# Kernel optimization log

Hardware: AMD Instinct MI355X
Metric: run time of the kernel (lower is better)

Reference implementation:

```python
import jax, jax.numpy as jnp
import numpy as np

VOCAB = 50001  # vocab_size + 1
EMB = 64
HID = 128
TAGS = 32
B, T = 256, 512


def setup_inputs() -> dict:
    key = jax.random.key(0)
    ks = jax.random.split(key, 12)
    inputs = jax.random.randint(ks[0], (B, T), 0, VOCAB)
    labels = jax.random.randint(ks[1], (B, T), 0, TAGS)
    E = jax.random.normal(ks[2], (VOCAB, EMB), jnp.float32) * 0.1
    def glorot(k, shape):
        fan = sum(shape)
        return jax.random.uniform(k, shape, jnp.float32, -1.0, 1.0) * jnp.sqrt(6.0 / fan)
    Wk_f = glorot(ks[3], (EMB, 4 * HID))
    Wr_f = glorot(ks[4], (HID, 4 * HID))
    b_f = jnp.zeros((4 * HID,), jnp.float32)
    Wk_b = glorot(ks[5], (EMB, 4 * HID))
    Wr_b = glorot(ks[6], (HID, 4 * HID))
    b_b = jnp.zeros((4 * HID,), jnp.float32)
    Wd = glorot(ks[7], (2 * HID, TAGS))
    bd = jnp.zeros((TAGS,), jnp.float32)
    transition = jax.random.uniform(ks[8], (TAGS, TAGS), jnp.float32)
    return {"inputs": inputs, "labels": labels, "E": E,
            "Wk_f": Wk_f, "Wr_f": Wr_f, "b_f": b_f,
            "Wk_b": Wk_b, "Wr_b": Wr_b, "b_b": b_b,
            "Wd": Wd, "bd": bd, "transition": transition}


def _lstm(x, Wk, Wr, b, reverse):
    # x: (B, T, D) -> (B, T, H); Keras gate order i, f, g(cell), o
    Bb = x.shape[0]
    H = Wr.shape[0]
    xs = jnp.swapaxes(x, 0, 1)  # (T, B, D)

    def step(carry, xt):
        h, c = carry
        z = xt @ Wk + h @ Wr + b
        i, f, g, o = jnp.split(z, 4, axis=-1)
        c = jax.nn.sigmoid(f) * c + jax.nn.sigmoid(i) * jnp.tanh(g)
        h = jax.nn.sigmoid(o) * jnp.tanh(c)
        return (h, c), h

    init = (jnp.zeros((Bb, H), x.dtype), jnp.zeros((Bb, H), x.dtype))
    _, hs = jax.lax.scan(step, init, xs, reverse=reverse)
    return jnp.swapaxes(hs, 0, 1)  # (B, T, H), time-aligned for both directions


def _crf_log_likelihood(logits, labels, transition):
    # logits: (B, T, K), labels: (B, T) int, full-length sequences
    lt = jnp.swapaxes(logits, 0, 1)  # (T, B, K)

    def fstep(alpha, lg):
        # alpha: (B, K) -> logsumexp over previous tag
        alpha = jax.nn.logsumexp(alpha[:, :, None] + transition[None], axis=1) + lg
        return alpha, None

    alpha, _ = jax.lax.scan(fstep, lt[0], lt[1:])
    log_norm = jax.nn.logsumexp(alpha, axis=-1)  # (B,)
    unary = jnp.take_along_axis(logits, labels[..., None], axis=-1)[..., 0].sum(-1)
    binary = transition[labels[:, :-1], labels[:, 1:]].sum(-1)
    return unary + binary - log_norm


def reference(inputs, labels, E, Wk_f, Wr_f, b_f, Wk_b, Wr_b, b_b, Wd, bd, transition):
    emb = E[inputs]  # (B, T, EMB) embedding lookup
    h_f = _lstm(emb, Wk_f, Wr_f, b_f, reverse=False)
    h_b = _lstm(emb, Wk_b, Wr_b, b_b, reverse=True)
    h = jnp.concatenate([h_f, h_b], axis=-1)  # (B, T, 2H)
    logits = h @ Wd + bd  # (B, T, K)
    log_likelihood = _crf_log_likelihood(logits, labels, transition)
    return log_likelihood, transition
```

## Files before the change

### kernel.cpp

```cpp
#include <hip/hip_runtime.h>
#include <hip/hip_bf16.h>
#include <cstdint>
#include <cstddef>

#define VOCAB 50001
#define EMB 64
#define HID 128
#define G4  512
#define TAGS 32
#define BATCH 256
#define SEQ 512

typedef _Float16 f16;
typedef _Float16 f16x2 __attribute__((ext_vector_type(2)));
typedef _Float16 f16x4 __attribute__((ext_vector_type(4)));
typedef _Float16 f16x8 __attribute__((ext_vector_type(8)));
typedef float f32x4 __attribute__((ext_vector_type(4)));

__device__ __forceinline__ float rcpf(float x) { return __builtin_amdgcn_rcpf(x); }

#define MFMA16(A, B, C) __builtin_amdgcn_mfma_f32_16x16x32_f16((A), (B), (C), 0, 0, 0)

__global__ __launch_bounds__(256)
void gtab_mfma_kernel(const float* __restrict__ E,
                      const float* __restrict__ Wk_f, const float* __restrict__ b_f,
                      const float* __restrict__ Wk_b, const float* __restrict__ b_b,
                      f16* __restrict__ G_f, f16* __restrict__ G_b) {
  const int dir = blockIdx.z;
  const float* __restrict__ Wk   = dir ? Wk_b : Wk_f;
  const float* __restrict__ bias = dir ? b_b  : b_f;
  f16* __restrict__ G = dir ? G_b : G_f;

  const int m0 = blockIdx.x * 64;
  const int n0 = blockIdx.y * 256;
  const int tid = threadIdx.x;

  __shared__ f16 Eh[64][80];
  __shared__ f16 Bh[256][80];

  #pragma unroll
  for (int s = 0; s < 4; ++s) {
    int idx = tid + s * 256;
    int r = idx >> 4, c4 = (idx & 15) * 4;
    int row = m0 + r;
    float4 ev;
    if (row < VOCAB) ev = *(const float4*)(E + (size_t)row * EMB + c4);
    else { ev.x = 0.f; ev.y = 0.f; ev.z = 0.f; ev.w = 0.f; }
    f16x4 v; v[0] = (f16)ev.x; v[1] = (f16)ev.y; v[2] = (f16)ev.z; v[3] = (f16)ev.w;
    *(f16x4*)&Eh[r][c4] = v;
  }
  #pragma unroll
  for (int s = 0; s < 32; ++s) {
    int idx = tid + s * 256;
    int k = idx >> 7, n2 = (idx & 127) * 2;
    float2 wv = *(const float2*)(Wk + (size_t)k * G4 + n0 + n2);
    Bh[n2][k]     = (f16)wv.x;
    Bh[n2 + 1][k] = (f16)wv.y;
  }
  __syncthreads();

  const int w = tid >> 6, l = tid & 63, mn = l & 15, q = l >> 4;
  f16x8 a0 = *(const f16x8*)&Eh[16 * w + mn][8 * q];
  f16x8 a1 = *(const f16x8*)&Eh[16 * w + mn][32 + 8 * q];

  f32x4 acc[16];
  #pragma unroll
  for (int nt = 0; nt < 16; ++nt) {
    f16x8 b0 = *(const f16x8*)&Bh[16 * nt + mn][8 * q];
    f16x8 b1 = *(const f16x8*)&Bh[16 * nt + mn][32 + 8 * q];
    f32x4 z = {0.f, 0.f, 0.f, 0.f};
    z = MFMA16(a0, b0, z);
    z = MFMA16(a1, b1, z);
    acc[nt] = z;
  }

  const int gA = n0 >> 7;
  #pragma unroll
  for (int nt = 0; nt < 8; ++nt) {
    int hid = 16 * nt + mn;
    float bv0 = bias[n0 + 16 * nt + mn];
    float bv1 = bias[n0 + 128 + 16 * nt + mn];
    #pragma unroll
    for (int reg = 0; reg < 4; ++reg) {
      int row = m0 + 16 * w + 4 * q + reg;
      if (row < VOCAB) {
        f16x2 v; v.x = (f16)(acc[nt][reg] + bv0); v.y = (f16)(acc[nt + 8][reg] + bv1);
        *(f16x2*)(G + (size_t)row * G4 + hid * 4 + gA) = v;
      }
    }
  }
}

__global__ __launch_bounds__(512, 1)
void lstm_mfma_kernel(const int* __restrict__ tokens,
                      const f16* __restrict__ G_f, const f16* __restrict__ G_b,
                      const float* __restrict__ Wr_f, const float* __restrict__ Wr_b,
                      const float* __restrict__ Wd, const float* __restrict__ bd,
                      float* __restrict__ Lf, float* __restrict__ Lb) {
  const int bg  = blockIdx.x;
  const int dir = blockIdx.y;
  const int b0  = bg * 2;
  const f16* __restrict__ G = dir ? G_b : G_f;
  const float* __restrict__ Wr = dir ? Wr_b : Wr_f;
  float* __restrict__ Lout = dir ? Lb : Lf;

  const int tid = threadIdx.x;
  const int w = tid >> 6;
  const int l = tid & 63;
  const int mn = l & 15;
  const int q  = l >> 4;
  const int hid = 16 * w + mn;

  __shared__ __align__(16) f16 h_lds[2][2][160];
  __shared__ int tokT[SEQ][2];

  tokT[tid][0] = tokens[(size_t)(b0 + 0) * SEQ + tid];
  tokT[tid][1] = tokens[(size_t)(b0 + 1) * SEQ + tid];
  if (tid < 160) ((unsigned*)&h_lds[0][0][0])[tid] = 0u;

  f16x8 bw[4][4];
  #pragma unroll
  for (int g = 0; g < 4; ++g) {
    #pragma unroll
    for (int s = 0; s < 4; ++s) {
      f16x8 v;
      const int colv = 128 * g + hid;
      #pragma unroll
      for (int j = 0; j < 8; ++j)
        v[j] = (f16)Wr[(size_t)(32 * s + 8 * q + j) * G4 + colv];
      bw[g][s] = v;
    }
  }
  f16x8 wdf0{}, wdf1{}, wdf2{}, wdf3{};
  float bdv = 0.0f;
  if (w >= 6) {
    const int tag = 16 * (w - 6) + mn;
    #pragma unroll
    for (int j = 0; j < 8; ++j) {
      wdf0[j] = (f16)Wd[(size_t)(128 * dir +  0 + 8 * q + j) * TAGS + tag];
      wdf1[j] = (f16)Wd[(size_t)(128 * dir + 32 + 8 * q + j) * TAGS + tag];
      wdf2[j] = (f16)Wd[(size_t)(128 * dir + 64 + 8 * q + j) * TAGS + tag];
      wdf3[j] = (f16)Wd[(size_t)(128 * dir + 96 + 8 * q + j) * TAGS + tag];
    }
    if (dir == 0) bdv = bd[tag];
  }

  float cst = 0.0f;
  __syncthreads();

#define TT(S) (dir ? (SEQ - 1 - (S)) : (S))

#define LOADG(S, GV) do { if (l < 32) {                                        \
    int _tk = tokT[TT(S)][q];                                                  \
    GV = *(const uint2*)(G + (size_t)_tk * G4 + hid * 4); } } while (0)

#define STEP(S, GV) do {                                                       \
    const int _s = (S);                                                        \
    const int _t = TT(_s);                                                     \
    const f16* hb = &h_lds[_s & 1][mn & 1][0];                                 \
    f16x8 a0 = *(const f16x8*)(hb      + 8 * q);                               \
    f16x8 a1 = *(const f16x8*)(hb + 32 + 8 * q);                               \
    f16x8 a2 = *(const f16x8*)(hb + 64 + 8 * q);                               \
    f16x8 a3 = *(const f16x8*)(hb + 96 + 8 * q);                               \
    f32x4 z0 = {0.f,0.f,0.f,0.f}, z1 = {0.f,0.f,0.f,0.f};                      \
    f32x4 z2 = {0.f,0.f,0.f,0.f}, z3 = {0.f,0.f,0.f,0.f};                      \
    z0 = MFMA16(a0, bw[0][0], z0); z0 = MFMA16(a1, bw[0][1], z0);              \
    z0 = MFMA16(a2, bw[0][2], z0); z0 = MFMA16(a3, bw[0][3], z0);              \
    z1 = MFMA16(a0, bw[1][0], z1); z1 = MFMA16(a1, bw[1][1], z1);              \
    z1 = MFMA16(a2, bw[1][2], z1); z1 = MFMA16(a3, bw[1][3], z1);              \
    z2 = MFMA16(a0, bw[2][0], z2); z2 = MFMA16(a1, bw[2][1], z2);              \
    z2 = MFMA16(a2, bw[2][2], z2); z2 = MFMA16(a3, bw[2][3], z2);              \
    z3 = MFMA16(a0, bw[3][0], z3); z3 = MFMA16(a1, bw[3][1], z3);              \
    z3 = MFMA16(a2, bw[3][2], z3); z3 = MFMA16(a3, bw[3][3], z3);              \
    if (w >= 6) {                                                              \
      f32x4 la = {0.f,0.f,0.f,0.f};                                            \
      la = MFMA16(a0, wdf0, la); la = MFMA16(a1, wdf1, la);                    \
      la = MFMA16(a2, wdf2, la); la = MFMA16(a3, wdf3, la);                    \
      if (q == 0) {                                                            \
        const int tag = 16 * (w - 6) + mn;                                     \
        Lout[((size_t)(b0 + 0) * SEQ + _t) * TAGS + tag] = la[0] + bdv;        \
        Lout[((size_t)(b0 + 1) * SEQ + _t) * TAGS + tag] = la[1] + bdv;        \
      }                                                                        \
    }                                                                          \
    float s0 = __shfl(z0[1], mn);                                              \
    float s1 = __shfl(z1[1], mn);                                              \
    float s2 = __shfl(z2[1], mn);                                              \
    float s3 = __shfl(z3[1], mn);                                              \
    if (l < 32) {                                                              \
      float zi = q ? s0 : z0[0];                                               \
      float zf = q ? s1 : z1[0];                                               \
      float zg = q ? s2 : z2[0];                                               \
      float zo = q ? s3 : z3[0];                                               \
      f16x4 gv = __builtin_bit_cast(f16x4, GV);                                \
      zi += (float)gv[0]; zf += (float)gv[1];                                  \
      zg += (float)gv[2]; zo += (float)gv[3];                                  \
      float ei = __expf(-zi);                                                  \
      float eg = __expf(fminf(2.f * zg, 30.f));                                \
      float sab = (eg - 1.f) * rcpf((1.f + ei) * (eg + 1.f));                  \
      float ef = __expf(-zf);                                                  \
      float cc = rcpf(1.f + ef) * cst + sab;                                   \
      cst = cc;                                                                \
      float eo = __expf(-zo);                                                  \
      float ec = __expf(fminf(2.f * cc, 30.f));                                \
      float hh = (ec - 1.f) * rcpf((1.f + eo) * (ec + 1.f));                   \
      h_lds[(_s + 1) & 1][q][hid] = (f16)hh;                                   \
    }                                                                          \
    asm volatile("s_waitcnt lgkmcnt(0)" ::: "memory");                         \
    __builtin_amdgcn_s_barrier();                                              \
  } while (0)

  uint2 gA, gB, gC, gD;
  LOADG(0, gA); LOADG(1, gB); LOADG(2, gC); LOADG(3, gD);

  for (int it = 0; it < SEQ / 4; ++it) {
    const int s = 4 * it;
    STEP(s + 0, gA);
    { int sc = (s + 4 < SEQ) ? s + 4 : SEQ - 1; LOADG(sc, gA); }
    STEP(s + 1, gB);
    { int sc = (s + 5 < SEQ) ? s + 5 : SEQ - 1; LOADG(sc, gB); }
    STEP(s + 2, gC);
    { int sc = (s + 6 < SEQ) ? s + 6 : SEQ - 1; LOADG(sc, gC); }
    STEP(s + 3, gD);
    { int sc = (s + 7 < SEQ) ? s + 7 : SEQ - 1; LOADG(sc, gD); }
  }
#undef STEP
#undef LOADG
#undef TT
}

__global__ __launch_bounds__(64)
void crf_kernel(const float* __restrict__ Lf,
                const float* __restrict__ Lb,
                const float* __restrict__ trans,
                const int* __restrict__ labels,
                float* __restrict__ out) {
  const int b = blockIdx.x;
  const int lane = threadIdx.x;
  const int k  = lane & 31;
  const int jh = lane >> 5;

  __shared__ float tr[TAGS * TAGS];
  __shared__ __align__(16) float e_lds[TAGS];

  for (int i = lane; i < TAGS * TAGS; i += 64) tr[i] = trans[i];
  __syncthreads();

  float wxp[16];
  #pragma unroll
  for (int i = 0; i < 16; ++i) wxp[i] = __expf(tr[(jh * 16 + i) * TAGS + k]);

  const size_t base0 = (size_t)b * SEQ * TAGS;
  float cur = Lf[base0 + k] + Lb[base0 + k];
  float beta0 = __shfl(cur, 0);
  float beta = cur - beta0;
  float S = beta0;

  float nxt = Lf[base0 + TAGS + k] + Lb[base0 + TAGS + k];

  for (int t = 1; t < SEQ; ++t) {
    float e = __expf(beta);
    if (lane < TAGS) e_lds[k] = e;
    asm volatile("s_waitcnt lgkmcnt(0)" ::: "memory");
    const float4* ep = (const float4*)&e_lds[jh * 16];
    float4 e0 = ep[0], e1 = ep[1], e2 = ep[2], e3 = ep[3];
    float d0 = e0.x * wxp[0]  + e0.y * wxp[1]  + e0.z * wxp[2]  + e0.w * wxp[3];
    float d1 = e1.x * wxp[4]  + e1.y * wxp[5]  + e1.z * wxp[6]  + e1.w * wxp[7];
    float d2 = e2.x * wxp[8]  + e2.y * wxp[9]  + e2.z * wxp[10] + e2.w * wxp[11];
    float d3 = e3.x * wxp[12] + e3.y * wxp[13] + e3.z * wxp[14] + e3.w * wxp[15];
    float dot = (d0 + d1) + (d2 + d3);
    dot += __shfl_xor(dot, 32);
    float braw = __logf(dot) + nxt;
    float bz = __shfl(braw, 0);
    beta = braw - bz;
    S += bz;
    if (t + 1 < SEQ) {
      size_t idx = base0 + (size_t)(t + 1) * TAGS + k;
      nxt = Lf[idx] + Lb[idx];
    }
  }

  float m = beta;
  #pragma unroll
  for (int off = 1; off <= 16; off <<= 1) m = fmaxf(m, __shfl_xor(m, off));
  float ex = (lane < TAGS) ? __expf(beta - m) : 0.0f;
  float s = ex;
  #pragma unroll
  for (int off = 1; off <= 32; off <<= 1) s += __shfl_xor(s, off);

  const int* lab = labels + (size_t)b * SEQ;
  float uacc = 0.f, bacc = 0.f;
  for (int t = lane; t < SEQ; t += 64) {
    int l0 = lab[t];
    size_t idx = base0 + (size_t)t * TAGS + l0;
    uacc += Lf[idx] + Lb[idx];
    if (t + 1 < SEQ) bacc += tr[l0 * TAGS + lab[t + 1]];
  }
  float red = uacc + bacc;
  #pragma unroll
  for (int off = 1; off <= 32; off <<= 1) red += __shfl_xor(red, off);

  if (lane == 0) out[b] = red - (m + __logf(s) + S);
}

__global__ void copy_trans_kernel(const float* __restrict__ trans,
                                  float* __restrict__ out) {
  int i = blockIdx.x * blockDim.x + threadIdx.x;
  if (i < TAGS * TAGS) out[i] = trans[i];
}

extern "C" void kernel_launch(void* const* d_in, const int* in_sizes, int n_in,
                              void* d_out, int out_size, void* d_ws, size_t ws_size,
                              hipStream_t stream) {
  const int*   inputs = (const int*)  d_in[0];
  const int*   labels = (const int*)  d_in[1];
  const float* E      = (const float*)d_in[2];
  const float* Wk_f   = (const float*)d_in[3];
  const float* Wr_f   = (const float*)d_in[4];
  const float* b_f    = (const float*)d_in[5];
  const float* Wk_b   = (const float*)d_in[6];
  const float* Wr_b   = (const float*)d_in[7];
  const float* b_b    = (const float*)d_in[8];
  const float* Wd     = (const float*)d_in[9];
  const float* bd     = (const float*)d_in[10];
  const float* trans  = (const float*)d_in[11];
  float* out = (float*)d_out;

  char* ws = (char*)d_ws;
  const size_t G_ELEMS = (size_t)VOCAB * G4;
  f16* G_f = (f16*)ws;
  f16* G_b = G_f + G_ELEMS;
  float* Lfp = (float*)(ws + 2 * G_ELEMS * sizeof(f16));
  float* Lbp = Lfp + (size_t)BATCH * SEQ * TAGS;

  dim3 ggrid((VOCAB + 63) / 64, 2, 2);
  gtab_mfma_kernel<<<ggrid, 256, 0, stream>>>(E, Wk_f, b_f, Wk_b, b_b, G_f, G_b);

  lstm_mfma_kernel<<<dim3(BATCH / 2, 2), 512, 0, stream>>>(
      inputs, G_f, G_b, Wr_f, Wr_b, Wd, bd, Lfp, Lbp);

  crf_kernel<<<BATCH, 64, 0, stream>>>(Lfp, Lbp, trans, labels, out);

  copy_trans_kernel<<<(TAGS * TAGS + 255) / 256, 256, 0, stream>>>(trans, out + BATCH);
}
```

Before: 526.5 us.

## Assign one batch row per LSTM block, doubling grid and allowing multiple blocks per CU

The LSTM kernel now handles one sequence per block instead of two, which doubles the grid to 512 blocks. Launch bounds are raised so up to four blocks can share a CU. Gate pre-activations are exchanged through shared memory with an extra barrier per step instead of cross-lane shuffles, and token offsets are pre-scaled to byte offsets. Because each MFMA now uses only one of its 16 rows, matrix-unit utilisation per block drops, and the added barrier lengthens the serial chain. The CRF kernel also swaps its lane-0 shuffle broadcasts for readfirstlane.

New measurement: 626.1 us. +18.9%, slower.

```diff
diff --git a/kernel.cpp b/kernel.cpp
--- a/kernel.cpp
+++ b/kernel.cpp
@@ -18,6 +18,9 @@
 typedef float f32x4 __attribute__((ext_vector_type(4)));
 
 __device__ __forceinline__ float rcpf(float x) { return __builtin_amdgcn_rcpf(x); }
+__device__ __forceinline__ float rfl(float x) {
+  return __builtin_bit_cast(float, __builtin_amdgcn_readfirstlane(__builtin_bit_cast(int, x)));
+}
 
 #define MFMA16(A, B, C) __builtin_amdgcn_mfma_f32_16x16x32_f16((A), (B), (C), 0, 0, 0)
 
@@ -91,16 +94,16 @@
   }
 }
 
-__global__ __launch_bounds__(512, 1)
+__global__ __launch_bounds__(512, 4)
 void lstm_mfma_kernel(const int* __restrict__ tokens,
                       const f16* __restrict__ G_f, const f16* __restrict__ G_b,
                       const float* __restrict__ Wr_f, const float* __restrict__ Wr_b,
                       const float* __restrict__ Wd, const float* __restrict__ bd,
                       float* __restrict__ Lf, float* __restrict__ Lb) {
-  const int bg  = blockIdx.x;
+  const int b   = blockIdx.x;
   const int dir = blockIdx.y;
-  const int b0  = bg * 2;
   const f16* __restrict__ G = dir ? G_b : G_f;
+  const char* __restrict__ Gc = (const char*)G;
   const float* __restrict__ Wr = dir ? Wr_b : Wr_f;
   float* __restrict__ Lout = dir ? Lb : Lf;
 
@@ -111,12 +114,12 @@
   const int q  = l >> 4;
   const int hid = 16 * w + mn;
 
-  __shared__ __align__(16) f16 h_lds[2][2][160];
-  __shared__ int tokT[SEQ][2];
-
-  tokT[tid][0] = tokens[(size_t)(b0 + 0) * SEQ + tid];
-  tokT[tid][1] = tokens[(size_t)(b0 + 1) * SEQ + tid];
-  if (tid < 160) ((unsigned*)&h_lds[0][0][0])[tid] = 0u;
+  __shared__ __align__(16) f16 h_lds[2][160];
+  __shared__ float z_lds[G4];
+  __shared__ int tokT[SEQ];
+
+  tokT[tid] = tokens[(size_t)b * SEQ + tid] << 10;
+  if (tid < 64) ((unsigned*)&h_lds[0][0])[tid] = 0u;
 
   f16x8 bw[4][4];
   #pragma unroll
@@ -150,14 +153,13 @@
 
 #define TT(S) (dir ? (SEQ - 1 - (S)) : (S))
 
-#define LOADG(S, GV) do { if (l < 32) {                                        \
-    int _tk = tokT[TT(S)][q];                                                  \
-    GV = *(const uint2*)(G + (size_t)_tk * G4 + hid * 4); } } while (0)
+#define LOADG(S, GV) do { if (tid < 128) {                                     \
+    GV = *(const uint2*)(Gc + tokT[TT(S)] + tid * 8); } } while (0)
 
 #define STEP(S, GV) do {                                                       \
     const int _s = (S);                                                        \
     const int _t = TT(_s);                                                     \
-    const f16* hb = &h_lds[_s & 1][mn & 1][0];                                 \
+    const f16* hb = &h_lds[_s & 1][0];                                         \
     f16x8 a0 = *(const f16x8*)(hb      + 8 * q);                               \
     f16x8 a1 = *(const f16x8*)(hb + 32 + 8 * q);                               \
     f16x8 a2 = *(const f16x8*)(hb + 64 + 8 * q);                               \
@@ -178,19 +180,22 @@
       la = MFMA16(a2, wdf2, la); la = MFMA16(a3, wdf3, la);                    \
       if (q == 0) {                                                            \
         const int tag = 16 * (w - 6) + mn;                                     \
-        Lout[((size_t)(b0 + 0) * SEQ + _t) * TAGS + tag] = la[0] + bdv;        \
-        Lout[((size_t)(b0 + 1) * SEQ + _t) * TAGS + tag] = la[1] + bdv;        \
+        Lout[((size_t)b * SEQ + _t) * TAGS + tag] = la[0] + bdv;               \
       }                                                                        \
     }                                                                          \
-    float s0 = __shfl(z0[1], mn);                                              \
-    float s1 = __shfl(z1[1], mn);                                              \
-    float s2 = __shfl(z2[1], mn);                                              \
-    float s3 = __shfl(z3[1], mn);                                              \
-    if (l < 32) {                                                              \
-      float zi = q ? s0 : z0[0];                                               \
-      float zf = q ? s1 : z1[0];                                               \
-      float zg = q ? s2 : z2[0];                                               \
-      float zo = q ? s3 : z3[0];                                               \
+    if (q == 0) {                                                              \
+      z_lds[      hid] = z0[0];                                                \
+      z_lds[128 + hid] = z1[0];                                                \
+      z_lds[256 + hid] = z2[0];                                                \
+      z_lds[384 + hid] = z3[0];                                                \
+    }                                                                          \
+    asm volatile("s_waitcnt lgkmcnt(0)" ::: "memory");                         \
+    __builtin_amdgcn_s_barrier();                                              \
+    if (tid < 128) {                                                           \
+      float zi = z_lds[      tid];                                             \
+      float zf = z_lds[128 + tid];                                             \
+      float zg = z_lds[256 + tid];                                             \
+      float zo = z_lds[384 + tid];                                             \
       f16x4 gv = __builtin_bit_cast(f16x4, GV);                                \
       zi += (float)gv[0]; zf += (float)gv[1];                                  \
       zg += (float)gv[2]; zo += (float)gv[3];                                  \
@@ -203,7 +208,7 @@
       float eo = __expf(-zo);                                                  \
       float ec = __expf(fminf(2.f * cc, 30.f));                                \
       float hh = (ec - 1.f) * rcpf((1.f + eo) * (ec + 1.f));                   \
-      h_lds[(_s + 1) & 1][q][hid] = (f16)hh;                                   \
+      h_lds[(_s + 1) & 1][tid] = (f16)hh;                                      \
     }                                                                          \
     asm volatile("s_waitcnt lgkmcnt(0)" ::: "memory");                         \
     __builtin_amdgcn_s_barrier();                                              \
@@ -251,7 +256,7 @@
 
   const size_t base0 = (size_t)b * SEQ * TAGS;
   float cur = Lf[base0 + k] + Lb[base0 + k];
-  float beta0 = __shfl(cur, 0);
+  float beta0 = rfl(cur);
   float beta = cur - beta0;
   float S = beta0;
 
@@ -270,7 +275,7 @@
     float dot = (d0 + d1) + (d2 + d3);
     dot += __shfl_xor(dot, 32);
     float braw = __logf(dot) + nxt;
-    float bz = __shfl(braw, 0);
+    float bz = rfl(braw);
     beta = braw - bz;
     S += bz;
     if (t + 1 < SEQ) {
@@ -335,7 +340,7 @@
   dim3 ggrid((VOCAB + 63) / 64, 2, 2);
   gtab_mfma_kernel<<<ggrid, 256, 0, stream>>>(E, Wk_f, b_f, Wk_b, b_b, G_f, G_b);
 
-  lstm_mfma_kernel<<<dim3(BATCH / 2, 2), 512, 0, stream>>>(
+  lstm_mfma_kernel<<<dim3(BATCH, 2), 512, 0, stream>>>(
       inputs, G_f, G_b, Wr_f, Wr_b, Wd, bd, Lfp, Lbp);
 
   crf_kernel<<<BATCH, 64, 0, stream>>>(Lfp, Lbp, trans, labels, out);
```

## Process four batch rows per LSTM block and use readfirstlane in CRF

Applied to the files above, without the earlier changes.

The LSTM kernel now handles four sequences per workgroup instead of two, filling all four MFMA accumulator rows. That halves the grid to 128 blocks, and every lane now does gate math, so the cross-lane shuffles are gone. Token indices are pre-scaled to byte offsets so the gate-table address needs less arithmetic. The CRF kernel replaces lane-0 shuffles with readfirstlane, which should be cheaper. The per-block serial step does more elementwise work, and fewer blocks may leave CUs idle (MI355X has 256 CUs).

After: 513.6 us. 1.03x faster.

```diff
diff --git a/kernel.cpp b/kernel.cpp
--- a/kernel.cpp
+++ b/kernel.cpp
@@ -18,6 +18,9 @@
 typedef float f32x4 __attribute__((ext_vector_type(4)));
 
 __device__ __forceinline__ float rcpf(float x) { return __builtin_amdgcn_rcpf(x); }
+__device__ __forceinline__ float rfl(float x) {
+  return __builtin_bit_cast(float, __builtin_amdgcn_readfirstlane(__builtin_bit_cast(int, x)));
+}
 
 #define MFMA16(A, B, C) __builtin_amdgcn_mfma_f32_16x16x32_f16((A), (B), (C), 0, 0, 0)
 
@@ -99,8 +102,9 @@
                       float* __restrict__ Lf, float* __restrict__ Lb) {
   const int bg  = blockIdx.x;
   const int dir = blockIdx.y;
-  const int b0  = bg * 2;
+  const int b0  = bg * 4;
   const f16* __restrict__ G = dir ? G_b : G_f;
+  const char* __restrict__ Gc = (const char*)G;
   const float* __restrict__ Wr = dir ? Wr_b : Wr_f;
   float* __restrict__ Lout = dir ? Lb : Lf;
 
@@ -110,13 +114,18 @@
   const int mn = l & 15;
   const int q  = l >> 4;
   const int hid = 16 * w + mn;
-
-  __shared__ __align__(16) f16 h_lds[2][2][160];
-  __shared__ int tokT[SEQ][2];
-
-  tokT[tid][0] = tokens[(size_t)(b0 + 0) * SEQ + tid];
-  tokT[tid][1] = tokens[(size_t)(b0 + 1) * SEQ + tid];
-  if (tid < 160) ((unsigned*)&h_lds[0][0][0])[tid] = 0u;
+  const int hid8 = hid * 8;
+
+  __shared__ __align__(16) f16 h_lds[2][4][160];
+  __shared__ int tokT[SEQ][4];
+
+  #pragma unroll
+  for (int s = 0; s < 4; ++s) {
+    int idx = tid + s * 512;
+    int t = idx >> 2, qq = idx & 3;
+    tokT[t][qq] = tokens[(size_t)(b0 + qq) * SEQ + t] << 10;
+  }
+  if (tid < 320) ((unsigned*)&h_lds[0][0][0])[tid] = 0u;
 
   f16x8 bw[4][4];
   #pragma unroll
@@ -150,14 +159,17 @@
 
 #define TT(S) (dir ? (SEQ - 1 - (S)) : (S))
 
-#define LOADG(S, GV) do { if (l < 32) {                                        \
+#define LOADG(S, GV) do {                                                      \
     int _tk = tokT[TT(S)][q];                                                  \
-    GV = *(const uint2*)(G + (size_t)_tk * G4 + hid * 4); } } while (0)
+    GV = *(const uint2*)(Gc + _tk + hid8);                                     \
+  } while (0)
+
+#define SEL4(V) ((q & 2) ? ((q & 1) ? V[3] : V[2]) : ((q & 1) ? V[1] : V[0]))
 
 #define STEP(S, GV) do {                                                       \
     const int _s = (S);                                                        \
     const int _t = TT(_s);                                                     \
-    const f16* hb = &h_lds[_s & 1][mn & 1][0];                                 \
+    const f16* hb = &h_lds[_s & 1][mn & 3][0];                                 \
     f16x8 a0 = *(const f16x8*)(hb      + 8 * q);                               \
     f16x8 a1 = *(const f16x8*)(hb + 32 + 8 * q);                               \
     f16x8 a2 = *(const f16x8*)(hb + 64 + 8 * q);                               \
@@ -180,17 +192,15 @@
         const int tag = 16 * (w - 6) + mn;                                     \
         Lout[((size_t)(b0 + 0) * SEQ + _t) * TAGS + tag] = la[0] + bdv;        \
         Lout[((size_t)(b0 + 1) * SEQ + _t) * TAGS + tag] = la[1] + bdv;        \
+        Lout[((size_t)(b0 + 2) * SEQ + _t) * TAGS + tag] = la[2] + bdv;        \
+        Lout[((size_t)(b0 + 3) * SEQ + _t) * TAGS + tag] = la[3] + bdv;        \
       }                                                                        \
     }                                                                          \
-    float s0 = __shfl(z0[1], mn);                                              \
-    float s1 = __shfl(z1[1], mn);                                              \
-    float s2 = __shfl(z2[1], mn);                                              \
-    float s3 = __shfl(z3[1], mn);                                              \
-    if (l < 32) {                                                              \
-      float zi = q ? s0 : z0[0];                                               \
-      float zf = q ? s1 : z1[0];                                               \
-      float zg = q ? s2 : z2[0];                                               \
-      float zo = q ? s3 : z3[0];                                               \
+    {                                                                          \
+      float zi = SEL4(z0);                                                     \
+      float zf = SEL4(z1);                                                     \
+      float zg = SEL4(z2);                                                     \
+      float zo = SEL4(z3);                                                     \
       f16x4 gv = __builtin_bit_cast(f16x4, GV);                                \
       zi += (float)gv[0]; zf += (float)gv[1];                                  \
       zg += (float)gv[2]; zo += (float)gv[3];                                  \
@@ -224,6 +234,7 @@
     { int sc = (s + 7 < SEQ) ? s + 7 : SEQ - 1; LOADG(sc, gD); }
   }
 #undef STEP
+#undef SEL4
 #undef LOADG
 #undef TT
 }
@@ -251,7 +262,7 @@
 
   const size_t base0 = (size_t)b * SEQ * TAGS;
   float cur = Lf[base0 + k] + Lb[base0 + k];
-  float beta0 = __shfl(cur, 0);
+  float beta0 = rfl(cur);
   float beta = cur - beta0;
   float S = beta0;
 
@@ -270,7 +281,7 @@
     float dot = (d0 + d1) + (d2 + d3);
     dot += __shfl_xor(dot, 32);
     float braw = __logf(dot) + nxt;
-    float bz = __shfl(braw, 0);
+    float bz = rfl(braw);
     beta = braw - bz;
     S += bz;
     if (t + 1 < SEQ) {
@@ -335,7 +346,7 @@
   dim3 ggrid((VOCAB + 63) / 64, 2, 2);
   gtab_mfma_kernel<<<ggrid, 256, 0, stream>>>(E, Wk_f, b_f, Wk_b, b_b, G_f, G_b);
 
-  lstm_mfma_kernel<<<dim3(BATCH / 2, 2), 512, 0, stream>>>(
+  lstm_mfma_kernel<<<dim3(BATCH / 4, 2), 512, 0, stream>>>(
       inputs, G_f, G_b, Wr_f, Wr_b, Wd, bd, Lfp, Lbp);
 
   crf_kernel<<<BATCH, 64, 0, stream>>>(Lfp, Lbp, trans, labels, out);
```
